# Performance work log

Measured on AMD Instinct MI355X. Metric: run time of the kernel, lower is better.

Reference implementation:

```python
import jax, jax.numpy as jnp
import numpy as np

B, N, C, K = 4, 4096, 64, 32   # graphs, points/graph, feat dim, max_neighbors
R = 0.2                         # radius
H1, H2, H3 = 64, 64, 128        # edge-MLP widths (nn = MLP([C+3, 64, 64, 128]))


def setup_inputs() -> dict:
    key = jax.random.key(0)
    ks = jax.random.split(key, 6)
    x = jax.random.normal(ks[0], (B * N, C), jnp.float32)
    pos = jax.random.uniform(ks[1], (B * N, 3), jnp.float32)  # unit cube
    batch = jnp.repeat(jnp.arange(B, dtype=jnp.int32), N)      # sorted, equal-size graphs
    W1 = jax.random.normal(ks[2], (C + 3, H1), jnp.float32) * 0.1
    b1 = jnp.zeros((H1,), jnp.float32)
    W2 = jax.random.normal(ks[3], (H1, H2), jnp.float32) * 0.1
    b2 = jnp.zeros((H2,), jnp.float32)
    W3 = jax.random.normal(ks[4], (H2, H3), jnp.float32) * 0.1
    b3 = jnp.zeros((H3,), jnp.float32)
    return dict(x=x, pos=pos, batch=batch, W1=W1, b1=b1, W2=W2, b2=b2, W3=W3, b3=b3)


def reference(x, pos, batch, W1, b1, W2, b2, W3, b3):
    # ratio == 1.0 -> idx = all points (identity sampling per the torch code).
    posb = pos.reshape(B, N, 3)
    xb = x.reshape(B, N, C)

    # radius neighbor search within each graph: squared pairwise distances [B, N_tgt, N_src]
    p2 = jnp.sum(posb * posb, axis=-1)                              # [B,N]
    d2 = p2[:, :, None] + p2[:, None, :] - 2.0 * jnp.einsum('bnd,bmd->bnm', posb, posb)
    score = jnp.where(d2 <= R * R, -d2, -jnp.inf)                   # valid -> nearest-first
    top, nb = jax.lax.top_k(score, K)                               # [B,N,K] K nearest in ball
    valid = jnp.isfinite(top)                                        # self (d2=0) always valid -> covers add_self_loops

    gather = jax.vmap(lambda arr, idx: arr[idx])                     # per-graph gather
    x_j = gather(xb, nb)                                             # [B,N,K,C]
    pos_j = gather(posb, nb)                                         # [B,N,K,3]
    rel = pos_j - posb[:, :, None, :]                                # pos_j - pos_i

    # PointNetConv message: h = nn([x_j, pos_j - pos_i]); nn = Lin+ReLU x3
    h = jnp.concatenate([x_j, rel], axis=-1)                         # [B,N,K,C+3]
    h = jax.nn.relu(h @ W1 + b1)
    h = jax.nn.relu(h @ W2 + b2)
    h = jax.nn.relu(h @ W3 + b3)                                     # [B,N,K,H3]

    # max aggregation over neighbors (PointNetConv default aggr='max')
    neg = jnp.finfo(h.dtype).min
    h = jnp.where(valid[..., None], h, neg)
    out = jnp.max(h, axis=2).reshape(B * N, H3)                      # [B*N, 128]

    return out, pos, batch
```

## Files before the change

kernel.cpp:

```cpp
#include <hip/hip_runtime.h>
#include <hip/hip_bf16.h>
#include <float.h>
#include <stdint.h>

#define NPTS 4096
#define NB_K 32
#define CAP  256

typedef short bf16x8 __attribute__((ext_vector_type(8)));
typedef float f32x4  __attribute__((ext_vector_type(4)));
#define MFMA_BF16 __builtin_amdgcn_mfma_f32_16x16x32_bf16
#define SCHED_FENCE() __builtin_amdgcn_sched_barrier(0)

__device__ __forceinline__ short bf16rne(float f) {
    unsigned u = __float_as_uint(f);
    unsigned r = u + 0x7fffu + ((u >> 16) & 1u);
    return (short)(r >> 16);
}
__device__ __forceinline__ short bfc(float f) {
    __hip_bfloat16 h = __float2bfloat16(f);
    return __builtin_bit_cast(short, h);
}

__global__ __launch_bounds__(256, 4) void knn_kernel(
    const float* __restrict__ x, const float* __restrict__ pos,
    const float* __restrict__ W1, const float* __restrict__ W2, const float* __restrict__ W3,
    unsigned short* __restrict__ nb16, short* __restrict__ frg, short* __restrict__ xb) {
    __shared__ int cand[8][CAP];
    const int tid = threadIdx.x;

    {
        const size_t base = ((size_t)blockIdx.x * 256 + tid) * 2;
        const float2 f = *(const float2*)(x + base);
        short2 o; o.x = bfc(f.x); o.y = bfc(f.y);
        *(short2*)(xb + base) = o;
    }

    if (blockIdx.x < 9) {
        const int t = blockIdx.x * 256 + tid;
        const int frag = t >> 6, lane = t & 63;
        const int col16 = lane & 15, kg = lane >> 4;
        bf16x8 v;
        if (frag < 12) {
            const int s = frag >> 2, n = frag & 3;
            #pragma unroll
            for (int j = 0; j < 8; ++j) {
                const int k = s * 32 + kg * 8 + j;
                v[j] = (k < 67) ? bf16rne(W1[k * 64 + n * 16 + col16]) : (short)0;
            }
        } else if (frag < 20) {
            const int s = (frag - 12) >> 2, n = (frag - 12) & 3;
            #pragma unroll
            for (int j = 0; j < 8; ++j) {
                const int k = (2 * s + (j >> 2)) * 16 + kg * 4 + (j & 3);
                v[j] = bf16rne(W2[k * 64 + n * 16 + col16]);
            }
        } else {
            const int s = (frag - 20) >> 3, n = (frag - 20) & 7;
            #pragma unroll
            for (int j = 0; j < 8; ++j) {
                const int k = (2 * s + (j >> 2)) * 16 + kg * 4 + (j & 3);
                v[j] = bf16rne(W3[k * 128 + n * 16 + col16]);
            }
        }
        *(bf16x8*)(frg + (size_t)t * 8) = v;
    }

    const int wv = tid >> 6, lane = tid & 63;
    const int tgtA = (blockIdx.x * 4 + wv) * 2;
    const int gb = tgtA & ~(NPTS - 1);
    const unsigned long long ltm = (1ull << lane) - 1ull;

    const float tAx = pos[(size_t)tgtA * 3 + 0];
    const float tAy = pos[(size_t)tgtA * 3 + 1];
    const float tAz = pos[(size_t)tgtA * 3 + 2];
    const float tBx = pos[(size_t)(tgtA + 1) * 3 + 0];
    const float tBy = pos[(size_t)(tgtA + 1) * 3 + 1];
    const float tBz = pos[(size_t)(tgtA + 1) * 3 + 2];
    const float RFILT = 0.040001f;

    int cntA = 0, cntB = 0;
    for (int c0 = 0; c0 < NPTS; c0 += 64) {
        const int j = c0 + lane;
        const float* pp = pos + (size_t)(gb + j) * 3;
        const float px = pp[0], py = pp[1], pz = pp[2];
        {
            const float dx = px - tAx, dy = py - tAy, dz = pz - tAz;
            const float d2 = fmaf(dx, dx, fmaf(dy, dy, dz * dz));
            const bool want = d2 <= RFILT;
            const unsigned long long m = __ballot(want);
            const int wp = cntA + __popcll(m & ltm);
            if (want && wp < CAP) cand[wv * 2][wp] = j;
            cntA += __popcll(m);
        }
        {
            const float dx = px - tBx, dy = py - tBy, dz = pz - tBz;
            const float d2 = fmaf(dx, dx, fmaf(dy, dy, dz * dz));
            const bool want = d2 <= RFILT;
            const unsigned long long m = __ballot(want);
            const int wp = cntB + __popcll(m & ltm);
            if (want && wp < CAP) cand[wv * 2 + 1][wp] = j;
            cntB += __popcll(m);
        }
    }
    if (cntA > CAP) cntA = CAP;
    if (cntB > CAP) cntB = CAP;

    const double RR = 0.2 * 0.2;
    const unsigned long long INF = ~0ull;

    for (int t = 0; t < 2; ++t) {
        const int tgt = tgtA + t;
        const int cnt = t ? cntB : cntA;
        const int* cd = cand[wv * 2 + t];
        const double txd = (double)pos[(size_t)tgt * 3 + 0];
        const double tyd = (double)pos[(size_t)tgt * 3 + 1];
        const double tzd = (double)pos[(size_t)tgt * 3 + 2];

        unsigned long long k0 = INF, k1 = INF, k2 = INF, k3 = INF;
#define LOADK(KS, S)                                                          \
        { const int p = lane + 64 * (S);                                      \
          if (p < cnt) {                                                      \
              const int ci = cd[p];                                           \
              const float* cp = pos + (size_t)(gb + ci) * 3;                  \
              const double ddx = (double)cp[0] - txd;                         \
              const double ddy = (double)cp[1] - tyd;                         \
              const double ddz = (double)cp[2] - tzd;                         \
              const double dd = fma(ddx, ddx, fma(ddy, ddy, ddz * ddz));      \
              if (dd <= RR)                                                   \
                  KS = ((unsigned long long)__double_as_longlong(dd)          \
                        & ~0xfffULL) | (unsigned long long)ci;                \
          } }
        LOADK(k0, 0) LOADK(k1, 1) LOADK(k2, 2) LOADK(k3, 3)
#undef LOADK

        const int cnt2 = __popcll(__ballot(k0 != INF)) + __popcll(__ballot(k1 != INF))
                       + __popcll(__ballot(k2 != INF)) + __popcll(__ballot(k3 != INF));

        unsigned long long pivot = 0xFFFFFFFFFFFFFFFEull;
        if (cnt2 > NB_K) {
            unsigned long long lo = 0, hi = 0x3FA5000000000000ull;
            for (int it = 0; it < 70; ++it) {
                const unsigned long long mid = lo + ((hi - lo) >> 1);
                const int c = __popcll(__ballot(k0 <= mid)) + __popcll(__ballot(k1 <= mid))
                            + __popcll(__ballot(k2 <= mid)) + __popcll(__ballot(k3 <= mid));
                if (c == NB_K) { pivot = mid; break; }
                if (c < NB_K) lo = mid + 1; else hi = mid - 1;
            }
        }

        int base = 0;
#define EMIT(KS)                                                              \
        { const bool sel = (KS <= pivot);                                     \
          const unsigned long long m = __ballot(sel);                         \
          const int wp = base + __popcll(m & ltm);                            \
          if (sel && wp < NB_K)                                               \
              nb16[(size_t)tgt * NB_K + wp] = (unsigned short)(KS & 0xfff);   \
          base += __popcll(m); }
        EMIT(k0) EMIT(k1) EMIT(k2) EMIT(k3)
#undef EMIT
        if (lane >= base && lane < NB_K)
            nb16[(size_t)tgt * NB_K + lane] = (unsigned short)0xFFFF;
    }
}

__global__ __launch_bounds__(256, 4) void mlp_kernel(
    const short* __restrict__ xb, const float* __restrict__ pos, const int* __restrict__ batch,
    const float* __restrict__ b1, const float* __restrict__ b2, const float* __restrict__ b3,
    const unsigned short* __restrict__ nb16, const short* __restrict__ frg,
    float* __restrict__ out) {
    __shared__ short bfr[36 * 64 * 8];

    const int tid = threadIdx.x, wv = tid >> 6, lane = tid & 63;

    for (int i = tid; i < 36 * 64; i += 256)
        *(bf16x8*)(bfr + (size_t)i * 8) = *(const bf16x8*)(frg + (size_t)i * 8);
    __syncthreads();

    const int c0 = lane & 15, kg = lane >> 4, rlow = kg * 4;
    const int wbase = blockIdx.x * 4 + wv;
    const int gb = (wbase * 4) & ~(NPTS - 1);

    int nvAll[2];
    #pragma unroll
    for (int q = 0; q < 2; ++q)
        nvAll[q] = (int)nb16[(size_t)(wbase * 4 + q * 2 + (lane >> 5)) * 32 + (lane & 31)];

    for (int p = 0; p < 4; ++p) {
        const int tgt = wbase * 4 + p;
        const int nv = nvAll[p >> 1];
        const unsigned long long bm = __ballot(nv != 0xFFFF);
        const unsigned vmask = (p & 1) ? (unsigned)(bm >> 32) : (unsigned)bm;

        int jrow[2];
        #pragma unroll
        for (int mm = 0; mm < 2; ++mm) {
            const int j = __shfl(nv, (p & 1) * 32 + mm * 16 + c0);
            jrow[mm] = (j == 0xFFFF) ? 0 : j;
        }

        bf16x8 X1[2][3];
        #pragma unroll
        for (int mm = 0; mm < 2; ++mm) {
            const short* xr = xb + (size_t)(gb + jrow[mm]) * 64;
            #pragma unroll
            for (int s = 0; s < 2; ++s)
                X1[mm][s] = *(const bf16x8*)(xr + s * 32 + kg * 8);
            bf16x8 a = {0, 0, 0, 0, 0, 0, 0, 0};
            if (kg == 0) {
                const float* pj = pos + (size_t)(gb + jrow[mm]) * 3;
                const float* pi = pos + (size_t)tgt * 3;
                a[0] = bfc(pj[0] - pi[0]);
                a[1] = bfc(pj[1] - pi[1]);
                a[2] = bfc(pj[2] - pi[2]);
            }
            X1[mm][2] = a;
        }

        bf16x8 B2[2][2];
        #pragma unroll
        for (int nt = 0; nt < 4; ++nt) {
            const float4 bb = *(const float4*)(b1 + nt * 16 + rlow);
            f32x4 acc[2];
            acc[0] = acc[1] = f32x4{bb.x, bb.y, bb.z, bb.w};
            #pragma unroll
            for (int s = 0; s < 3; ++s) {
                const bf16x8 Wf = *(const bf16x8*)(bfr + (size_t)((s * 4 + nt) * 64 + lane) * 8);
                #pragma unroll
                for (int mm = 0; mm < 2; ++mm)
                    acc[mm] = MFMA_BF16(Wf, X1[mm][s], acc[mm], 0, 0, 0);
            }
            #pragma unroll
            for (int mm = 0; mm < 2; ++mm)
                #pragma unroll
                for (int r = 0; r < 4; ++r)
                    B2[mm][nt >> 1][(nt & 1) * 4 + r] = bfc(fmaxf(acc[mm][r], 0.f));
            SCHED_FENCE();
        }

        bf16x8 A3[2][2];
        #pragma unroll
        for (int nt = 0; nt < 4; ++nt) {
            const float4 bb = *(const float4*)(b2 + nt * 16 + rlow);
            f32x4 acc[2];
            acc[0] = acc[1] = f32x4{bb.x, bb.y, bb.z, bb.w};
            #pragma unroll
            for (int s = 0; s < 2; ++s) {
                const bf16x8 Wf = *(const bf16x8*)(bfr + (size_t)((12 + s * 4 + nt) * 64 + lane) * 8);
                #pragma unroll
                for (int mm = 0; mm < 2; ++mm)
                    acc[mm] = MFMA_BF16(Wf, B2[mm][s], acc[mm], 0, 0, 0);
            }
            #pragma unroll
            for (int mm = 0; mm < 2; ++mm)
                #pragma unroll
                for (int r = 0; r < 4; ++r)
                    A3[mm][nt >> 1][(nt & 1) * 4 + r] = bfc(fmaxf(acc[mm][r], 0.f));
            SCHED_FENCE();
        }

        #pragma unroll
        for (int n = 0; n < 8; ++n) {
            const float bv = b3[n * 16 + c0];
            f32x4 acc[2];
            acc[0] = acc[1] = f32x4{bv, bv, bv, bv};
            #pragma unroll
            for (int s = 0; s < 2; ++s) {
                const bf16x8 Bf = *(const bf16x8*)(bfr + (size_t)((20 + s * 8 + n) * 64 + lane) * 8);
                #pragma unroll
                for (int mm = 0; mm < 2; ++mm)
                    acc[mm] = MFMA_BF16(A3[mm][s], Bf, acc[mm], 0, 0, 0);
            }
            float v = 0.f;
            #pragma unroll
            for (int mm = 0; mm < 2; ++mm)
                #pragma unroll
                for (int r = 0; r < 4; ++r) {
                    const int row = mm * 16 + rlow + r;
                    const float h = fmaxf(acc[mm][r], 0.f);
                    v = fmaxf(v, ((vmask >> row) & 1u) ? h : 0.f);
                }
            v = fmaxf(v, __shfl_xor(v, 16));
            v = fmaxf(v, __shfl_xor(v, 32));
            if (lane < 16) out[(size_t)tgt * 128 + n * 16 + lane] = v;
            SCHED_FENCE();
        }

        if (lane < 3)  out[2097152 + (size_t)tgt * 3 + lane] = pos[(size_t)tgt * 3 + lane];
        if (lane == 3) out[2146304 + tgt] = (float)batch[tgt];
    }
}

extern "C" void kernel_launch(void* const* d_in, const int* in_sizes, int n_in,
                              void* d_out, int out_size, void* d_ws, size_t ws_size,
                              hipStream_t stream) {
    const float* x   = (const float*)d_in[0];
    const float* pos = (const float*)d_in[1];
    const int* batch = (const int*)d_in[2];
    const float* W1  = (const float*)d_in[3];
    const float* b1  = (const float*)d_in[4];
    const float* W2  = (const float*)d_in[5];
    const float* b2  = (const float*)d_in[6];
    const float* W3  = (const float*)d_in[7];
    const float* b3  = (const float*)d_in[8];
    float* out = (float*)d_out;

    short* xb = (short*)d_ws;
    unsigned short* nb16 = (unsigned short*)((char*)d_ws + (2 << 20));
    short* frg = (short*)((char*)d_ws + (3 << 20));

    hipLaunchKernelGGL(knn_kernel, dim3(2048), dim3(256), 0, stream,
                       x, pos, W1, W2, W3, nb16, frg, xb);
    hipLaunchKernelGGL(mlp_kernel, dim3(1024), dim3(256), 0, stream,
                       xb, pos, batch, b1, b2, b3, nb16, frg, out);
}
```

Measured before the change: 77.55 us.

## Bin points into per-graph xy grid columns to prune radius neighbor scan

Adds a binning kernel that assigns each point to a 5x5 xy column per graph with atomic counters and writes column-sorted positions and original indices. The kNN kernel then scans only the columns overlapping the target's radius box instead of all 4096 points in the graph, cutting the distance filtering work. Weight fragment prep and the bf16 conversion of x move into separate small kernels, so there are now two extra launches. Columns hold at most 320 points, so points beyond that would be silently dropped for clustered inputs.

```diff
diff --git a/kernel.cpp b/kernel.cpp
--- a/kernel.cpp
+++ b/kernel.cpp
@@ -6,6 +6,7 @@
 #define NPTS 4096
 #define NB_K 32
 #define CAP  256
+#define CAPC 320
 
 typedef short bf16x8 __attribute__((ext_vector_type(8)));
 typedef float f32x4  __attribute__((ext_vector_type(4)));
@@ -22,114 +23,146 @@
     return __builtin_bit_cast(short, h);
 }
 
-__global__ __launch_bounds__(256, 4) void knn_kernel(
-    const float* __restrict__ x, const float* __restrict__ pos,
-    const float* __restrict__ W1, const float* __restrict__ W2, const float* __restrict__ W3,
-    unsigned short* __restrict__ nb16, short* __restrict__ frg, short* __restrict__ xb) {
+__global__ __launch_bounds__(256) void prep0_kernel(const float* __restrict__ W1,
+                                                    const float* __restrict__ W2,
+                                                    const float* __restrict__ W3,
+                                                    short* __restrict__ frg,
+                                                    unsigned* __restrict__ cnt) {
+    const int tid = threadIdx.x;
+    if (blockIdx.x == 9) {
+        if (tid < 100) cnt[tid] = 0;
+        return;
+    }
+    const int t = blockIdx.x * 256 + tid;
+    const int frag = t >> 6, lane = t & 63;
+    const int col16 = lane & 15, kg = lane >> 4;
+    bf16x8 v;
+    if (frag < 12) {
+        const int s = frag >> 2, n = frag & 3;
+        #pragma unroll
+        for (int j = 0; j < 8; ++j) {
+            const int k = s * 32 + kg * 8 + j;
+            v[j] = (k < 67) ? bf16rne(W1[k * 64 + n * 16 + col16]) : (short)0;
+        }
+    } else if (frag < 20) {
+        const int s = (frag - 12) >> 2, n = (frag - 12) & 3;
+        #pragma unroll
+        for (int j = 0; j < 8; ++j) {
+            const int k = (2 * s + (j >> 2)) * 16 + kg * 4 + (j & 3);
+            v[j] = bf16rne(W2[k * 64 + n * 16 + col16]);
+        }
+    } else {
+        const int s = (frag - 20) >> 3, n = (frag - 20) & 7;
+        #pragma unroll
+        for (int j = 0; j < 8; ++j) {
+            const int k = (2 * s + (j >> 2)) * 16 + kg * 4 + (j & 3);
+            v[j] = bf16rne(W3[k * 128 + n * 16 + col16]);
+        }
+    }
+    *(bf16x8*)(frg + (size_t)t * 8) = v;
+}
+
+__global__ __launch_bounds__(256) void bin_kernel(const float* __restrict__ x,
+                                                  const float* __restrict__ pos,
+                                                  short* __restrict__ xb,
+                                                  float* __restrict__ possrt,
+                                                  unsigned short* __restrict__ sidx,
+                                                  unsigned* __restrict__ cnt) {
+    const int id = blockIdx.x * 256 + threadIdx.x;
+
+    #pragma unroll
+    for (int r = 0; r < 8; ++r) {
+        const size_t base = (size_t)r * 131072 + (size_t)id * 8;
+        const float4 a = *(const float4*)(x + base);
+        const float4 b = *(const float4*)(x + base + 4);
+        bf16x8 o;
+        o[0] = bfc(a.x); o[1] = bfc(a.y); o[2] = bfc(a.z); o[3] = bfc(a.w);
+        o[4] = bfc(b.x); o[5] = bfc(b.y); o[6] = bfc(b.z); o[7] = bfc(b.w);
+        *(bf16x8*)(xb + base) = o;
+    }
+
+    const int g = id >> 12;
+    const float px = pos[(size_t)id * 3 + 0];
+    const float py = pos[(size_t)id * 3 + 1];
+    const float pz = pos[(size_t)id * 3 + 2];
+    int cx = (int)(px * 5.f); if (cx > 4) cx = 4;
+    int cy = (int)(py * 5.f); if (cy > 4) cy = 4;
+    const int col = g * 25 + cx * 5 + cy;
+    const unsigned slot = atomicAdd(&cnt[col], 1u);
+    if (slot < CAPC) {
+        const int li = col * CAPC + (int)slot;
+        possrt[(size_t)li * 3 + 0] = px;
+        possrt[(size_t)li * 3 + 1] = py;
+        possrt[(size_t)li * 3 + 2] = pz;
+        sidx[li] = (unsigned short)(id & (NPTS - 1));
+    }
+}
+
+__global__ __launch_bounds__(256, 4) void knn_kernel(const float* __restrict__ pos,
+                                                     const float* __restrict__ possrt,
+                                                     const unsigned short* __restrict__ sidx,
+                                                     const unsigned* __restrict__ cntArr,
+                                                     unsigned short* __restrict__ nb16) {
     __shared__ int cand[8][CAP];
     const int tid = threadIdx.x;
-
-    {
-        const size_t base = ((size_t)blockIdx.x * 256 + tid) * 2;
-        const float2 f = *(const float2*)(x + base);
-        short2 o; o.x = bfc(f.x); o.y = bfc(f.y);
-        *(short2*)(xb + base) = o;
-    }
-
-    if (blockIdx.x < 9) {
-        const int t = blockIdx.x * 256 + tid;
-        const int frag = t >> 6, lane = t & 63;
-        const int col16 = lane & 15, kg = lane >> 4;
-        bf16x8 v;
-        if (frag < 12) {
-            const int s = frag >> 2, n = frag & 3;
-            #pragma unroll
-            for (int j = 0; j < 8; ++j) {
-                const int k = s * 32 + kg * 8 + j;
-                v[j] = (k < 67) ? bf16rne(W1[k * 64 + n * 16 + col16]) : (short)0;
-            }
-        } else if (frag < 20) {
-            const int s = (frag - 12) >> 2, n = (frag - 12) & 3;
-            #pragma unroll
-            for (int j = 0; j < 8; ++j) {
-                const int k = (2 * s + (j >> 2)) * 16 + kg * 4 + (j & 3);
-                v[j] = bf16rne(W2[k * 64 + n * 16 + col16]);
-            }
-        } else {
-            const int s = (frag - 20) >> 3, n = (frag - 20) & 7;
-            #pragma unroll
-            for (int j = 0; j < 8; ++j) {
-                const int k = (2 * s + (j >> 2)) * 16 + kg * 4 + (j & 3);
-                v[j] = bf16rne(W3[k * 128 + n * 16 + col16]);
-            }
-        }
-        *(bf16x8*)(frg + (size_t)t * 8) = v;
-    }
-
     const int wv = tid >> 6, lane = tid & 63;
     const int tgtA = (blockIdx.x * 4 + wv) * 2;
-    const int gb = tgtA & ~(NPTS - 1);
+    const int g = tgtA >> 12;
     const unsigned long long ltm = (1ull << lane) - 1ull;
-
-    const float tAx = pos[(size_t)tgtA * 3 + 0];
-    const float tAy = pos[(size_t)tgtA * 3 + 1];
-    const float tAz = pos[(size_t)tgtA * 3 + 2];
-    const float tBx = pos[(size_t)(tgtA + 1) * 3 + 0];
-    const float tBy = pos[(size_t)(tgtA + 1) * 3 + 1];
-    const float tBz = pos[(size_t)(tgtA + 1) * 3 + 2];
     const float RFILT = 0.040001f;
-
-    int cntA = 0, cntB = 0;
-    for (int c0 = 0; c0 < NPTS; c0 += 64) {
-        const int j = c0 + lane;
-        const float* pp = pos + (size_t)(gb + j) * 3;
-        const float px = pp[0], py = pp[1], pz = pp[2];
-        {
-            const float dx = px - tAx, dy = py - tAy, dz = pz - tAz;
-            const float d2 = fmaf(dx, dx, fmaf(dy, dy, dz * dz));
-            const bool want = d2 <= RFILT;
-            const unsigned long long m = __ballot(want);
-            const int wp = cntA + __popcll(m & ltm);
-            if (want && wp < CAP) cand[wv * 2][wp] = j;
-            cntA += __popcll(m);
-        }
-        {
-            const float dx = px - tBx, dy = py - tBy, dz = pz - tBz;
-            const float d2 = fmaf(dx, dx, fmaf(dy, dy, dz * dz));
-            const bool want = d2 <= RFILT;
-            const unsigned long long m = __ballot(want);
-            const int wp = cntB + __popcll(m & ltm);
-            if (want && wp < CAP) cand[wv * 2 + 1][wp] = j;
-            cntB += __popcll(m);
-        }
-    }
-    if (cntA > CAP) cntA = CAP;
-    if (cntB > CAP) cntB = CAP;
-
     const double RR = 0.2 * 0.2;
     const unsigned long long INF = ~0ull;
 
     for (int t = 0; t < 2; ++t) {
         const int tgt = tgtA + t;
-        const int cnt = t ? cntB : cntA;
-        const int* cd = cand[wv * 2 + t];
-        const double txd = (double)pos[(size_t)tgt * 3 + 0];
-        const double tyd = (double)pos[(size_t)tgt * 3 + 1];
-        const double tzd = (double)pos[(size_t)tgt * 3 + 2];
-
+        const float tx = pos[(size_t)tgt * 3 + 0];
+        const float ty = pos[(size_t)tgt * 3 + 1];
+        const float tz = pos[(size_t)tgt * 3 + 2];
+
+        int cxl = (int)floorf((tx - 0.2001f) * 5.f); if (cxl < 0) cxl = 0;
+        int cxh = (int)floorf((tx + 0.2001f) * 5.f); if (cxh > 4) cxh = 4;
+        int cyl = (int)floorf((ty - 0.2001f) * 5.f); if (cyl < 0) cyl = 0;
+        int cyh = (int)floorf((ty + 0.2001f) * 5.f); if (cyh > 4) cyh = 4;
+
+        int* cd = cand[wv * 2 + t];
+        int cnt = 0;
+        for (int cx = cxl; cx <= cxh; ++cx)
+            for (int cy = cyl; cy <= cyh; ++cy) {
+                const int col = g * 25 + cx * 5 + cy;
+                int n = (int)cntArr[col]; if (n > CAPC) n = CAPC;
+                const int base = col * CAPC;
+                for (int s0 = 0; s0 < n; s0 += 64) {
+                    const int sl = s0 + lane;
+                    bool want = false;
+                    const int li = base + sl;
+                    if (sl < n) {
+                        const float* cp = possrt + (size_t)li * 3;
+                        const float dx = cp[0] - tx, dy = cp[1] - ty, dz = cp[2] - tz;
+                        const float d2 = fmaf(dx, dx, fmaf(dy, dy, dz * dz));
+                        want = d2 <= RFILT;
+                    }
+                    const unsigned long long m = __ballot(want);
+                    const int wp = cnt + __popcll(m & ltm);
+                    if (want && wp < CAP) cd[wp] = li;
+                    cnt += __popcll(m);
+                }
+            }
+        if (cnt > CAP) cnt = CAP;
+
+        const double txd = (double)tx, tyd = (double)ty, tzd = (double)tz;
         unsigned long long k0 = INF, k1 = INF, k2 = INF, k3 = INF;
 #define LOADK(KS, S)                                                          \
         { const int p = lane + 64 * (S);                                      \
           if (p < cnt) {                                                      \
-              const int ci = cd[p];                                           \
-              const float* cp = pos + (size_t)(gb + ci) * 3;                  \
+              const int li = cd[p];                                           \
+              const float* cp = possrt + (size_t)li * 3;                      \
               const double ddx = (double)cp[0] - txd;                         \
               const double ddy = (double)cp[1] - tyd;                         \
               const double ddz = (double)cp[2] - tzd;                         \
               const double dd = fma(ddx, ddx, fma(ddy, ddy, ddz * ddz));      \
               if (dd <= RR)                                                   \
                   KS = ((unsigned long long)__double_as_longlong(dd)          \
-                        & ~0xfffULL) | (unsigned long long)ci;                \
+                        & ~0xfffULL) | (unsigned long long)sidx[li];          \
           } }
         LOADK(k0, 0) LOADK(k1, 1) LOADK(k2, 2) LOADK(k3, 3)
 #undef LOADK
@@ -305,12 +338,17 @@
     const float* b3  = (const float*)d_in[8];
     float* out = (float*)d_out;
 
-    short* xb = (short*)d_ws;
-    unsigned short* nb16 = (unsigned short*)((char*)d_ws + (2 << 20));
-    short* frg = (short*)((char*)d_ws + (3 << 20));
-
-    hipLaunchKernelGGL(knn_kernel, dim3(2048), dim3(256), 0, stream,
-                       x, pos, W1, W2, W3, nb16, frg, xb);
+    char* ws = (char*)d_ws;
+    short* xb            = (short*)ws;
+    unsigned short* nb16 = (unsigned short*)(ws + (2 << 20));
+    short* frg           = (short*)(ws + (3 << 20));
+    unsigned* cnt        = (unsigned*)(ws + (3 << 20) + (64 << 10));
+    unsigned short* sidx = (unsigned short*)(ws + (3 << 20) + (128 << 10));
+    float* possrt        = (float*)(ws + (3 << 20) + (256 << 10));
+
+    hipLaunchKernelGGL(prep0_kernel, dim3(10), dim3(256), 0, stream, W1, W2, W3, frg, cnt);
+    hipLaunchKernelGGL(bin_kernel, dim3(64), dim3(256), 0, stream, x, pos, xb, possrt, sidx, cnt);
+    hipLaunchKernelGGL(knn_kernel, dim3(2048), dim3(256), 0, stream, pos, possrt, sidx, cnt, nb16);
     hipLaunchKernelGGL(mlp_kernel, dim3(1024), dim3(256), 0, stream,
                        xb, pos, batch, b1, b2, b3, nb16, frg, out);
 }
```

Result: slower. 98.48 us (+27.0%).
